# Performance work log

Measured on AMD Instinct MI355X. Metric: run time of the kernel, lower is better.

## Reference

```python
import jax, jax.numpy as jnp
import numpy as np

N_SEG = 128      # number of ragged segments (len(leng))
TOTAL = 32768    # total rows = sum(leng)
D = 1280         # cnn_feature (tf_efficientnet_b0 classifier.in_features)
D_HEAD = 512     # hidden of logits head


def setup_inputs() -> dict:
    key = jax.random.key(0)
    ks = jax.random.split(key, 8)
    # ragged lengths (static at trace time), summing exactly to TOTAL
    rng = np.random.default_rng(0)
    leng = rng.integers(64, 448, size=N_SEG).astype(np.int64)
    leng = np.maximum((leng * (TOTAL / leng.sum())).astype(np.int64), 1)
    leng[-1] += TOTAL - leng.sum()
    segment_ids = jnp.asarray(np.repeat(np.arange(N_SEG), leng), jnp.int32)

    features = jax.random.normal(ks[0], (TOTAL, D), jnp.float32)
    s = 0.02
    Ww = jax.random.normal(ks[1], (D, D), jnp.float32) * s        # proj_w.weight
    bw = jnp.zeros((D,), jnp.float32)                              # proj_w.bias
    v = jax.random.normal(ks[2], (D,), jnp.float32) * s           # proj_v.weight (1,D) squeezed
    W1 = jax.random.normal(ks[3], (D_HEAD, D), jnp.float32) * s   # logits[0].weight
    b1 = jnp.zeros((D_HEAD,), jnp.float32)
    W2 = jax.random.normal(ks[4], (1, D_HEAD), jnp.float32) * s   # logits[3].weight
    b2 = jnp.zeros((1,), jnp.float32)
    return {"features": features, "Ww": Ww, "bw": bw, "v": v,
            "W1": W1, "b1": b1, "W2": W2, "b2": b2,
            "segment_ids": segment_ids}


def reference(features, Ww, bw, v, W1, b1, W2, b2, segment_ids):
    # per-row attention logits: tanh(x @ Ww^T + bw) @ v    -> [TOTAL]
    H = jnp.tanh(features @ Ww.T + bw)
    s = H @ v
    # segment-wise stable softmax (replaces Python loop over leng)
    m = jax.ops.segment_max(s, segment_ids, num_segments=N_SEG)
    e = jnp.exp(s - m[segment_ids])
    z = jax.ops.segment_sum(e, segment_ids, num_segments=N_SEG)
    att = e / z[segment_ids]                                      # [TOTAL]
    # attention-weighted sum pooling per segment -> [N_SEG, D]
    pooled = jax.ops.segment_sum(features * att[:, None], segment_ids,
                                 num_segments=N_SEG)
    # logits head (dropout is identity in eval)
    h = jax.nn.relu(pooled @ W1.T + b1)
    return h @ W2.T + b2                                          # [N_SEG, 1]
```

## Files before the change

kernel.cpp:

```cpp
#include <hip/hip_runtime.h>
#include <hip/hip_bf16.h>


#define TOTAL_ROWS 32768
#define DIM 1280
#define NSEG 128
#define DHEAD 512

typedef _Float16 f16x8 __attribute__((ext_vector_type(8)));
typedef float f32x4 __attribute__((ext_vector_type(4)));

#define OFF_XH   0
#define OFF_WH   83886080
#define OFF_S    87162880
#define OFF_ATT  87293952
#define OFF_SEG  87425024
#define OFF_POOL 87426048
#define OFF_H    88081408

__device__ __forceinline__ void load_lds16(const void* g, void* l) {
  __builtin_amdgcn_global_load_lds(
      (const __attribute__((address_space(1))) unsigned int*)g,
      (__attribute__((address_space(3))) unsigned int*)l, 16, 0, 0);
}

__device__ __forceinline__ float tanh_fast(float x) {
  float e = __expf(2.0f * x);
  return 1.0f - 2.0f * __builtin_amdgcn_rcpf(e + 1.0f);
}

__global__ void cvt_f16_kernel(const float* __restrict__ a, _Float16* __restrict__ oa,
                               int na8, const float* __restrict__ b,
                               _Float16* __restrict__ ob, int nb8) {
  int i = blockIdx.x * blockDim.x + threadIdx.x;
  const float* in;
  _Float16* out;
  int idx;
  if (i < na8) {
    in = a; out = oa; idx = i;
  } else {
    idx = i - na8;
    if (idx >= nb8) return;
    in = b; out = ob;
  }
  const float4* p = (const float4*)in + (size_t)idx * 2;
  float4 u0 = p[0], u1 = p[1];
  f16x8 h;
  h[0] = (_Float16)u0.x; h[1] = (_Float16)u0.y;
  h[2] = (_Float16)u0.z; h[3] = (_Float16)u0.w;
  h[4] = (_Float16)u1.x; h[5] = (_Float16)u1.y;
  h[6] = (_Float16)u1.z; h[7] = (_Float16)u1.w;
  *((f16x8*)out + idx) = h;
}

__global__ void segstart_kernel(const int* __restrict__ sid,
                                int* __restrict__ segstart, int total) {
  int i = blockIdx.x * blockDim.x + threadIdx.x;
  if (i >= total) return;
  int sg = sid[i];
  if (i == 0) segstart[0] = 0;
  else if (sid[i - 1] != sg) segstart[sg] = i;
  if (i == total - 1) segstart[sg + 1] = total;
}

__global__ __launch_bounds__(256) void gemm_s_kernel(
    const _Float16* __restrict__ X, const _Float16* __restrict__ W,
    const float* __restrict__ v, const float* __restrict__ bw,
    float* __restrict__ s) {
  __shared__ _Float16 As[128 * 64];
  __shared__ _Float16 Bs[128 * 64];
  const int rowBase = blockIdx.x * 128;
  const int jBase = blockIdx.y * 128;
  const int t = threadIdx.x;
  const int lane = t & 63;
  const int w = t >> 6;
  const int wm = w & 1, wn = w >> 1;
  const int kc = lane >> 4;

  int aoff[2][4], boff[2][4];
#pragma unroll
  for (int s2 = 0; s2 < 2; ++s2) {
    int q = s2 * 4 + kc;
#pragma unroll
    for (int mt = 0; mt < 4; ++mt) {
      int rowA = wm * 64 + mt * 16 + (lane & 15);
      aoff[s2][mt] = rowA * 64 + ((q + rowA) & 7) * 8;
      int rowB = wn * 64 + mt * 16 + (lane & 15);
      boff[s2][mt] = rowB * 64 + ((q + rowB) & 7) * 8;
    }
  }
  const _Float16* gA[4];
  const _Float16* gB[4];
  const _Float16* lA[4];
  const _Float16* lB[4];
#pragma unroll
  for (int q = 0; q < 4; ++q) {
    int l = w * 256 + q * 64 + lane;
    int row = l >> 3;
    int g = ((l & 7) - row) & 7;
    gA[q] = X + (size_t)(rowBase + row) * DIM + g * 8;
    gB[q] = W + (size_t)(jBase + row) * DIM + g * 8;
    lA[q] = &As[(w * 256 + q * 64) * 8];
    lB[q] = &Bs[(w * 256 + q * 64) * 8];
  }

  f32x4 acc[4][4];
  const f32x4 zero = {0.f, 0.f, 0.f, 0.f};
#pragma unroll
  for (int i = 0; i < 4; ++i)
#pragma unroll
    for (int j = 0; j < 4; ++j) acc[i][j] = zero;

  for (int k0 = 0; k0 < DIM; k0 += 64) {
    __syncthreads();
#pragma unroll
    for (int q = 0; q < 4; ++q) {
      load_lds16(gA[q], (void*)lA[q]);
      load_lds16(gB[q], (void*)lB[q]);
      gA[q] += 64;
      gB[q] += 64;
    }
    __syncthreads();

    f16x8 a[2][4], b[2][4];
#pragma unroll
    for (int s2 = 0; s2 < 2; ++s2)
#pragma unroll
      for (int mt = 0; mt < 4; ++mt) {
        a[s2][mt] = *(const f16x8*)&As[aoff[s2][mt]];
        b[s2][mt] = *(const f16x8*)&Bs[boff[s2][mt]];
      }
#pragma unroll
    for (int s2 = 0; s2 < 2; ++s2)
#pragma unroll
      for (int mt = 0; mt < 4; ++mt)
#pragma unroll
        for (int nt = 0; nt < 4; ++nt)
          acc[mt][nt] = __builtin_amdgcn_mfma_f32_16x16x32_f16(
              a[s2][mt], b[s2][nt], acc[mt][nt], 0, 0, 0);
  }

  const int colBase = jBase + wn * 64 + (lane & 15);
  float vv[4], bb[4];
#pragma unroll
  for (int nt = 0; nt < 4; ++nt) {
    int j = colBase + nt * 16;
    vv[nt] = v[j];
    bb[nt] = bw[j];
  }
  const int g = lane >> 4;
#pragma unroll
  for (int mt = 0; mt < 4; ++mt) {
#pragma unroll
    for (int r = 0; r < 4; ++r) {
      float sumv = 0.f;
#pragma unroll
      for (int nt = 0; nt < 4; ++nt)
        sumv += tanh_fast(acc[mt][nt][r] + bb[nt]) * vv[nt];
      sumv += __shfl_xor(sumv, 1);
      sumv += __shfl_xor(sumv, 2);
      sumv += __shfl_xor(sumv, 4);
      sumv += __shfl_xor(sumv, 8);
      if ((lane & 15) == 0) {
        int row = rowBase + wm * 64 + mt * 16 + g * 4 + r;
        atomicAdd(&s[row], sumv);
      }
    }
  }
}

__global__ void softmax_kernel(const float* __restrict__ s,
                               const int* __restrict__ segstart,
                               float* __restrict__ att) {
  int seg = blockIdx.x;
  int st = segstart[seg], en = segstart[seg + 1];
  int t = threadIdx.x;
  __shared__ float red[8];
  float m = -1e30f;
  for (int i = st + t; i < en; i += 256) m = fmaxf(m, s[i]);
  for (int d = 1; d < 64; d <<= 1) m = fmaxf(m, __shfl_xor(m, d));
  if ((t & 63) == 0) red[t >> 6] = m;
  __syncthreads();
  m = fmaxf(fmaxf(red[0], red[1]), fmaxf(red[2], red[3]));
  float z = 0.f;
  for (int i = st + t; i < en; i += 256) z += __expf(s[i] - m);
  for (int d = 1; d < 64; d <<= 1) z += __shfl_xor(z, d);
  if ((t & 63) == 0) red[4 + (t >> 6)] = z;
  __syncthreads();
  z = red[4] + red[5] + red[6] + red[7];
  float rz = 1.0f / z;
  for (int i = st + t; i < en; i += 256) att[i] = __expf(s[i] - m) * rz;
}

__global__ void pool_kernel(const float* __restrict__ F,
                            const float* __restrict__ att,
                            const int* __restrict__ segstart,
                            float* __restrict__ pooled) {
  int seg = blockIdx.x, part = blockIdx.y;
  int st = segstart[seg], en = segstart[seg + 1];
  int len = en - st;
  int chunk = (len + 3) >> 2;
  int r0 = st + chunk * part;
  int r1 = min(en, r0 + chunk);
  int t = threadIdx.x;
  f32x4 acc = {0.f, 0.f, 0.f, 0.f};
  int r = r0;
  for (; r + 2 <= r1; r += 2) {
    float a0 = att[r], a1 = att[r + 1];
    f32x4 f0 = ((const f32x4*)(F + (size_t)r * DIM))[t];
    f32x4 f1 = ((const f32x4*)(F + (size_t)(r + 1) * DIM))[t];
#pragma unroll
    for (int c = 0; c < 4; ++c) {
      acc[c] = fmaf(a0, f0[c], acc[c]);
      acc[c] = fmaf(a1, f1[c], acc[c]);
    }
  }
  if (r < r1) {
    float a0 = att[r];
    f32x4 f0 = ((const f32x4*)(F + (size_t)r * DIM))[t];
#pragma unroll
    for (int c = 0; c < 4; ++c) acc[c] = fmaf(a0, f0[c], acc[c]);
  }
  float* dst = pooled + (size_t)seg * DIM + t * 4;
#pragma unroll
  for (int c = 0; c < 4; ++c) atomicAdd(dst + c, acc[c]);
}

__global__ void head1_kernel(const float* __restrict__ pooled,
                             const float* __restrict__ W1,
                             const float* __restrict__ b1, float* __restrict__ h) {
  int og = blockIdx.x, sg = blockIdx.y;
  __shared__ float Wt[16 * 65];
  __shared__ float Pt[32 * 65];
  int t = threadIdx.x;
  int tx = t & 15, ty = t >> 4;
  float acc0 = 0.f, acc1 = 0.f;
  for (int kcc = 0; kcc < 20; ++kcc) {
    __syncthreads();
#pragma unroll
    for (int u = 0; u < 4; ++u) {
      int lin = t + 256 * u;
      int o = lin >> 6, kk = lin & 63;
      Wt[o * 65 + kk] = W1[(size_t)(og * 16 + o) * DIM + kcc * 64 + kk];
    }
#pragma unroll
    for (int u = 0; u < 8; ++u) {
      int lin = t + 256 * u;
      int ss = lin >> 6, kk = lin & 63;
      Pt[ss * 65 + kk] = pooled[(size_t)(sg * 32 + ss) * DIM + kcc * 64 + kk];
    }
    __syncthreads();
#pragma unroll
    for (int kk = 0; kk < 64; ++kk) {
      float wv = Wt[tx * 65 + kk];
      acc0 = fmaf(Pt[ty * 65 + kk], wv, acc0);
      acc1 = fmaf(Pt[(ty + 16) * 65 + kk], wv, acc1);
    }
  }
  int o = og * 16 + tx;
  float bias = b1[o];
  h[(size_t)(sg * 32 + ty) * DHEAD + o] = fmaxf(acc0 + bias, 0.f);
  h[(size_t)(sg * 32 + ty + 16) * DHEAD + o] = fmaxf(acc1 + bias, 0.f);
}

__global__ void head2_kernel(const float* __restrict__ h,
                             const float* __restrict__ W2,
                             const float* __restrict__ b2, float* __restrict__ out) {
  int seg = blockIdx.x;
  int t = threadIdx.x;
  float val = h[(size_t)seg * DHEAD + t] * W2[t] +
              h[(size_t)seg * DHEAD + t + 256] * W2[t + 256];
  for (int d = 1; d < 64; d <<= 1) val += __shfl_xor(val, d);
  __shared__ float red[4];
  if ((t & 63) == 0) red[t >> 6] = val;
  __syncthreads();
  if (t == 0) out[seg] = red[0] + red[1] + red[2] + red[3] + b2[0];
}

extern "C" void kernel_launch(void* const* d_in, const int* in_sizes, int n_in,
                              void* d_out, int out_size, void* d_ws, size_t ws_size,
                              hipStream_t stream) {
  const float* features = (const float*)d_in[0];
  const float* Ww = (const float*)d_in[1];
  const float* bw = (const float*)d_in[2];
  const float* v = (const float*)d_in[3];
  const float* W1 = (const float*)d_in[4];
  const float* b1 = (const float*)d_in[5];
  const float* W2 = (const float*)d_in[6];
  const float* b2 = (const float*)d_in[7];
  const int* segids = (const int*)d_in[8];
  float* out = (float*)d_out;

  char* ws = (char*)d_ws;
  _Float16* Xh = (_Float16*)(ws + OFF_XH);
  _Float16* Wh = (_Float16*)(ws + OFF_WH);
  float* s = (float*)(ws + OFF_S);
  float* att = (float*)(ws + OFF_ATT);
  int* segstart = (int*)(ws + OFF_SEG);
  float* pooled = (float*)(ws + OFF_POOL);
  float* h = (float*)(ws + OFF_H);

  hipMemsetAsync(s, 0, TOTAL_ROWS * sizeof(float), stream);
  hipMemsetAsync(pooled, 0, NSEG * DIM * sizeof(float), stream);

  const int na8 = TOTAL_ROWS * DIM / 8;
  const int nb8 = DIM * DIM / 8;
  cvt_f16_kernel<<<(na8 + nb8 + 255) / 256, 256, 0, stream>>>(features, Xh, na8,
                                                              Ww, Wh, nb8);
  segstart_kernel<<<TOTAL_ROWS / 256, 256, 0, stream>>>(segids, segstart, TOTAL_ROWS);

  dim3 ggrid(TOTAL_ROWS / 128, DIM / 128);
  gemm_s_kernel<<<ggrid, 256, 0, stream>>>(Xh, Wh, v, bw, s);

  softmax_kernel<<<NSEG, 256, 0, stream>>>(s, segstart, att);
  pool_kernel<<<dim3(NSEG, 4), 320, 0, stream>>>(features, att, segstart, pooled);
  head1_kernel<<<dim3(32, 4), 256, 0, stream>>>(pooled, W1, b1, h);
  head2_kernel<<<NSEG, 256, 0, stream>>>(h, W2, b2, out);
}
```

Measured before the change: 495.7 us.

## Pool from fp16 features, fold memsets into kernels, slim GEMM addressing

The pooling kernel now reads the fp16 copy of the features that already exists, halving the bytes it pulls from memory, and its grid is split into 8 row chunks per segment instead of 4. The two memset calls are removed: the segstart kernel zeroes the score buffer and the softmax kernel zeroes the pooled rows. The GEMM recomputes LDS and global offsets from a few base values, which cuts register use, and it interleaves fragment loads with MFMAs per k-substep. Pooling on fp16 features adds rounding error to the pooled output.

New measurement: 476.5 us. 1.04x faster.

```diff
diff --git a/kernel.cpp b/kernel.cpp
--- a/kernel.cpp
+++ b/kernel.cpp
@@ -8,6 +8,7 @@
 #define DHEAD 512
 
 typedef _Float16 f16x8 __attribute__((ext_vector_type(8)));
+typedef _Float16 f16x4 __attribute__((ext_vector_type(4)));
 typedef float f32x4 __attribute__((ext_vector_type(4)));
 
 #define OFF_XH   0
@@ -54,9 +55,11 @@
 }
 
 __global__ void segstart_kernel(const int* __restrict__ sid,
-                                int* __restrict__ segstart, int total) {
+                                int* __restrict__ segstart, float* __restrict__ s,
+                                int total) {
   int i = blockIdx.x * blockDim.x + threadIdx.x;
   if (i >= total) return;
+  s[i] = 0.f;
   int sg = sid[i];
   if (i == 0) segstart[0] = 0;
   else if (sid[i - 1] != sg) segstart[sg] = i;
@@ -76,33 +79,20 @@
   const int w = t >> 6;
   const int wm = w & 1, wn = w >> 1;
   const int kc = lane >> 4;
-
-  int aoff[2][4], boff[2][4];
+  const int lm = lane & 15;
+
+  int aBase[2], bBase[2];
 #pragma unroll
   for (int s2 = 0; s2 < 2; ++s2) {
-    int q = s2 * 4 + kc;
-#pragma unroll
-    for (int mt = 0; mt < 4; ++mt) {
-      int rowA = wm * 64 + mt * 16 + (lane & 15);
-      aoff[s2][mt] = rowA * 64 + ((q + rowA) & 7) * 8;
-      int rowB = wn * 64 + mt * 16 + (lane & 15);
-      boff[s2][mt] = rowB * 64 + ((q + rowB) & 7) * 8;
-    }
-  }
-  const _Float16* gA[4];
-  const _Float16* gB[4];
-  const _Float16* lA[4];
-  const _Float16* lB[4];
-#pragma unroll
-  for (int q = 0; q < 4; ++q) {
-    int l = w * 256 + q * 64 + lane;
-    int row = l >> 3;
-    int g = ((l & 7) - row) & 7;
-    gA[q] = X + (size_t)(rowBase + row) * DIM + g * 8;
-    gB[q] = W + (size_t)(jBase + row) * DIM + g * 8;
-    lA[q] = &As[(w * 256 + q * 64) * 8];
-    lB[q] = &Bs[(w * 256 + q * 64) * 8];
-  }
+    int swz = ((kc + s2 * 4 + lm) & 7) * 8;
+    aBase[s2] = (wm * 64 + lm) * 64 + swz;
+    bBase[s2] = (wn * 64 + lm) * 64 + swz;
+  }
+
+  const int subrow = lane >> 3;
+  const int g = ((lane & 7) - subrow) & 7;
+  const _Float16* gA = X + (size_t)(rowBase + w * 32 + subrow) * DIM + g * 8;
+  const _Float16* gB = W + (size_t)(jBase + w * 32 + subrow) * DIM + g * 8;
 
   f32x4 acc[4][4];
   const f32x4 zero = {0.f, 0.f, 0.f, 0.f};
@@ -115,32 +105,29 @@
     __syncthreads();
 #pragma unroll
     for (int q = 0; q < 4; ++q) {
-      load_lds16(gA[q], (void*)lA[q]);
-      load_lds16(gB[q], (void*)lB[q]);
-      gA[q] += 64;
-      gB[q] += 64;
+      load_lds16(gA + k0 + q * (8 * DIM), &As[(w * 256 + q * 64) * 8]);
+      load_lds16(gB + k0 + q * (8 * DIM), &Bs[(w * 256 + q * 64) * 8]);
     }
     __syncthreads();
 
-    f16x8 a[2][4], b[2][4];
-#pragma unroll
-    for (int s2 = 0; s2 < 2; ++s2)
+#pragma unroll
+    for (int s2 = 0; s2 < 2; ++s2) {
+      f16x8 a[4], b[4];
 #pragma unroll
       for (int mt = 0; mt < 4; ++mt) {
-        a[s2][mt] = *(const f16x8*)&As[aoff[s2][mt]];
-        b[s2][mt] = *(const f16x8*)&Bs[boff[s2][mt]];
+        a[mt] = *(const f16x8*)&As[aBase[s2] + mt * 1024];
+        b[mt] = *(const f16x8*)&Bs[bBase[s2] + mt * 1024];
       }
-#pragma unroll
-    for (int s2 = 0; s2 < 2; ++s2)
 #pragma unroll
       for (int mt = 0; mt < 4; ++mt)
 #pragma unroll
         for (int nt = 0; nt < 4; ++nt)
           acc[mt][nt] = __builtin_amdgcn_mfma_f32_16x16x32_f16(
-              a[s2][mt], b[s2][nt], acc[mt][nt], 0, 0, 0);
-  }
-
-  const int colBase = jBase + wn * 64 + (lane & 15);
+              a[mt], b[nt], acc[mt][nt], 0, 0, 0);
+    }
+  }
+
+  const int colBase = jBase + wn * 64 + lm;
   float vv[4], bb[4];
 #pragma unroll
   for (int nt = 0; nt < 4; ++nt) {
@@ -148,7 +135,7 @@
     vv[nt] = v[j];
     bb[nt] = bw[j];
   }
-  const int g = lane >> 4;
+  const int gq = lane >> 4;
 #pragma unroll
   for (int mt = 0; mt < 4; ++mt) {
 #pragma unroll
@@ -161,8 +148,8 @@
       sumv += __shfl_xor(sumv, 2);
       sumv += __shfl_xor(sumv, 4);
       sumv += __shfl_xor(sumv, 8);
-      if ((lane & 15) == 0) {
-        int row = rowBase + wm * 64 + mt * 16 + g * 4 + r;
+      if (lm == 0) {
+        int row = rowBase + wm * 64 + mt * 16 + gq * 4 + r;
         atomicAdd(&s[row], sumv);
       }
     }
@@ -171,10 +158,12 @@
 
 __global__ void softmax_kernel(const float* __restrict__ s,
                                const int* __restrict__ segstart,
-                               float* __restrict__ att) {
+                               float* __restrict__ att,
+                               float* __restrict__ pooled) {
   int seg = blockIdx.x;
   int st = segstart[seg], en = segstart[seg + 1];
   int t = threadIdx.x;
+  for (int c = t; c < DIM; c += 256) pooled[(size_t)seg * DIM + c] = 0.f;
   __shared__ float red[8];
   float m = -1e30f;
   for (int i = st + t; i < en; i += 256) m = fmaxf(m, s[i]);
@@ -192,34 +181,34 @@
   for (int i = st + t; i < en; i += 256) att[i] = __expf(s[i] - m) * rz;
 }
 
-__global__ void pool_kernel(const float* __restrict__ F,
+__global__ void pool_kernel(const _Float16* __restrict__ F,
                             const float* __restrict__ att,
                             const int* __restrict__ segstart,
                             float* __restrict__ pooled) {
   int seg = blockIdx.x, part = blockIdx.y;
   int st = segstart[seg], en = segstart[seg + 1];
   int len = en - st;
-  int chunk = (len + 3) >> 2;
+  int chunk = (len + 7) >> 3;
   int r0 = st + chunk * part;
   int r1 = min(en, r0 + chunk);
   int t = threadIdx.x;
-  f32x4 acc = {0.f, 0.f, 0.f, 0.f};
+  float acc[4] = {0.f, 0.f, 0.f, 0.f};
   int r = r0;
   for (; r + 2 <= r1; r += 2) {
     float a0 = att[r], a1 = att[r + 1];
-    f32x4 f0 = ((const f32x4*)(F + (size_t)r * DIM))[t];
-    f32x4 f1 = ((const f32x4*)(F + (size_t)(r + 1) * DIM))[t];
+    f16x4 f0 = ((const f16x4*)(F + (size_t)r * DIM))[t];
+    f16x4 f1 = ((const f16x4*)(F + (size_t)(r + 1) * DIM))[t];
 #pragma unroll
     for (int c = 0; c < 4; ++c) {
-      acc[c] = fmaf(a0, f0[c], acc[c]);
-      acc[c] = fmaf(a1, f1[c], acc[c]);
+      acc[c] = fmaf(a0, (float)f0[c], acc[c]);
+      acc[c] = fmaf(a1, (float)f1[c], acc[c]);
     }
   }
   if (r < r1) {
     float a0 = att[r];
-    f32x4 f0 = ((const f32x4*)(F + (size_t)r * DIM))[t];
-#pragma unroll
-    for (int c = 0; c < 4; ++c) acc[c] = fmaf(a0, f0[c], acc[c]);
+    f16x4 f0 = ((const f16x4*)(F + (size_t)r * DIM))[t];
+#pragma unroll
+    for (int c = 0; c < 4; ++c) acc[c] = fmaf(a0, (float)f0[c], acc[c]);
   }
   float* dst = pooled + (size_t)seg * DIM + t * 4;
 #pragma unroll
@@ -300,20 +289,18 @@
   float* pooled = (float*)(ws + OFF_POOL);
   float* h = (float*)(ws + OFF_H);
 
-  hipMemsetAsync(s, 0, TOTAL_ROWS * sizeof(float), stream);
-  hipMemsetAsync(pooled, 0, NSEG * DIM * sizeof(float), stream);
-
   const int na8 = TOTAL_ROWS * DIM / 8;
   const int nb8 = DIM * DIM / 8;
   cvt_f16_kernel<<<(na8 + nb8 + 255) / 256, 256, 0, stream>>>(features, Xh, na8,
                                                               Ww, Wh, nb8);
-  segstart_kernel<<<TOTAL_ROWS / 256, 256, 0, stream>>>(segids, segstart, TOTAL_ROWS);
+  segstart_kernel<<<TOTAL_ROWS / 256, 256, 0, stream>>>(segids, segstart, s,
+                                                        TOTAL_ROWS);
 
   dim3 ggrid(TOTAL_ROWS / 128, DIM / 128);
   gemm_s_kernel<<<ggrid, 256, 0, stream>>>(Xh, Wh, v, bw, s);
 
-  softmax_kernel<<<NSEG, 256, 0, stream>>>(s, segstart, att);
-  pool_kernel<<<dim3(NSEG, 4), 320, 0, stream>>>(features, att, segstart, pooled);
+  softmax_kernel<<<NSEG, 256, 0, stream>>>(s, segstart, att, pooled);
+  pool_kernel<<<dim3(NSEG, 8), 320, 0, stream>>>(Xh, att, segstart, pooled);
   head1_kernel<<<dim3(32, 4), 256, 0, stream>>>(pooled, W1, b1, h);
   head2_kernel<<<NSEG, 256, 0, stream>>>(h, W2, b2, out);
 }
```
